# Performance work log

Measured on AMD Instinct MI355X. Metric: run time of the kernel, lower is better.

The kernel has to match this reference:

```python
import jax, jax.numpy as jnp
import numpy as np

# Config constants (mirror NEATConfig)
B = 4096          # population_size
N = 256           # nodes per genome (padded)
E = 4096          # connections per genome (padded)
NUM_INPUTS = 64
NUM_OUTPUTS = 8
NUM_LAYERS = 4    # layers 0..3; layer 0 = inputs


def setup_inputs() -> dict:
    key = jax.random.key(0)
    k_in, k_layer, k_ci, k_co, k_w, k_en = jax.random.split(key, 6)
    inputs = jax.random.normal(k_in, (B, NUM_INPUTS), dtype=jnp.float32)
    # first NUM_INPUTS nodes are input nodes (layer 0); rest in layers 1..NUM_LAYERS-1
    hidden_layers = jax.random.randint(k_layer, (B, N - NUM_INPUTS), 1, NUM_LAYERS, dtype=jnp.int32)
    node_layer = jnp.concatenate(
        [jnp.zeros((B, NUM_INPUTS), dtype=jnp.int32), hidden_layers], axis=1)
    conn_in = jax.random.randint(k_ci, (B, E), 0, N, dtype=jnp.int32)
    conn_out = jax.random.randint(k_co, (B, E), 0, N, dtype=jnp.int32)
    conn_weight = jax.random.normal(k_w, (B, E), dtype=jnp.float32)
    conn_enabled = jax.random.randint(k_en, (B, E), 0, 2) > 0
    return {
        "inputs": inputs,
        "node_layer": node_layer,
        "conn_in": conn_in,
        "conn_out": conn_out,
        "conn_weight": conn_weight,
        "conn_enabled": conn_enabled,
    }


def reference(inputs, node_layer, conn_in, conn_out, conn_weight, conn_enabled):
    """Batched NEAT.forward: layered gather-weight-sum-activate over connection graph.

    inputs:       [B, NUM_INPUTS] float
    node_layer:   [B, N] int  (layer id per node)
    conn_in/out:  [B, E] int  (connection endpoints)
    conn_weight:  [B, E] float
    conn_enabled: [B, E] bool
    returns:      [B, NUM_OUTPUTS]
    """
    b, n = node_layer.shape
    dtype = inputs.dtype
    enabled_f = conn_enabled.astype(dtype)
    batch_idx = jnp.arange(b)[:, None]  # [B,1] for batched scatter

    # node_values init: zeros, inputs written into first NUM_INPUTS slots
    vals = jnp.zeros((b, n), dtype=dtype).at[:, :NUM_INPUTS].set(inputs)

    # per-node count of enabled incoming connections (the `if not incoming: continue` mask)
    in_count = jnp.zeros((b, n), dtype=dtype).at[batch_idx, conn_out].add(enabled_f)

    for layer in range(1, NUM_LAYERS):
        # gather source values, weight, mask disabled -> messages [B,E]
        msgs = jnp.take_along_axis(vals, conn_in, axis=1) * conn_weight * enabled_f
        # sum-aggregate messages per target node [B,N]
        agg = jnp.zeros((b, n), dtype=dtype).at[batch_idx, conn_out].add(msgs)
        upd = jnp.tanh(agg)  # activation_default = tanh
        mask = (node_layer == layer) & (in_count > 0)
        vals = jnp.where(mask, upd, vals)

    return vals[:, NUM_INPUTS:NUM_INPUTS + NUM_OUTPUTS]
```

## Files before the change

### kernel.cpp

```cpp
#include <hip/hip_runtime.h>


#define NN   256
#define NE   4096
#define NIN  64
#define NOUT 8
#define NT   256
#define NWAVE 4

__global__ __launch_bounds__(NT) void neat_fwd(
    const float* __restrict__ inputs,
    const int*   __restrict__ node_layer,
    const int*   __restrict__ conn_in,
    const int*   __restrict__ conn_out,
    const float* __restrict__ conn_w,
    const unsigned char* __restrict__ conn_en,
    float*       __restrict__ out)
{
    const int b    = blockIdx.x;
    const int t    = threadIdx.x;
    const int wave = t >> 6;
    const int lane = t & 63;
    const unsigned long long lmlt = (1ull << lane) - 1ull;

    __shared__ float vals[NN];
    __shared__ float agg[NN];
    __shared__ int   nl_sh[NN];
    __shared__ uint2 edges[NE];
    __shared__ int   wave_cnt[NWAVE][3];
    __shared__ int   wave_base[NWAVE][3];
    __shared__ int   Loff[5];

    const unsigned int* en_w = (const unsigned int*)conn_en;
    bool byte_mode = false;
#pragma unroll
    for (int i = 0; i < 16; ++i) byte_mode |= (en_w[i] > 1u);

    const int nl = node_layer[(size_t)b * NN + t];
    nl_sh[t] = nl;
    vals[t]  = (t < NIN) ? inputs[(size_t)b * NIN + t] : 0.0f;

    const int4*   ci4 = (const int4*)(conn_in  + (size_t)b * NE);
    const int4*   co4 = (const int4*)(conn_out + (size_t)b * NE);
    const float4* w4  = (const float4*)(conn_w  + (size_t)b * NE);

    int4 a0 = ci4[t             ];
    int4 a1 = ci4[t + 1*NT      ];
    int4 a2 = ci4[t + 2*NT      ];
    int4 a3 = ci4[t + 3*NT      ];
    int4 c0 = co4[t             ];
    int4 c1 = co4[t + 1*NT      ];
    int4 c2 = co4[t + 2*NT      ];
    int4 c3 = co4[t + 3*NT      ];
    float4 w0 = w4[t            ];
    float4 w1 = w4[t + 1*NT     ];
    float4 w2 = w4[t + 2*NT     ];
    float4 w3 = w4[t + 3*NT     ];

    unsigned m = 0;
    if (byte_mode) {
        const uchar4* e4 = (const uchar4*)(conn_en + (size_t)b * NE);
        uchar4 e0 = e4[t       ];
        uchar4 e1 = e4[t + 1*NT];
        uchar4 e2 = e4[t + 2*NT];
        uchar4 e3 = e4[t + 3*NT];
        m = (e0.x ? 1u<<0  : 0u) | (e0.y ? 1u<<1  : 0u) | (e0.z ? 1u<<2  : 0u) | (e0.w ? 1u<<3  : 0u)
          | (e1.x ? 1u<<4  : 0u) | (e1.y ? 1u<<5  : 0u) | (e1.z ? 1u<<6  : 0u) | (e1.w ? 1u<<7  : 0u)
          | (e2.x ? 1u<<8  : 0u) | (e2.y ? 1u<<9  : 0u) | (e2.z ? 1u<<10 : 0u) | (e2.w ? 1u<<11 : 0u)
          | (e3.x ? 1u<<12 : 0u) | (e3.y ? 1u<<13 : 0u) | (e3.z ? 1u<<14 : 0u) | (e3.w ? 1u<<15 : 0u);
    } else {
        const int4* e4 = (const int4*)((const int*)conn_en + (size_t)b * NE);
        int4 e0 = e4[t       ];
        int4 e1 = e4[t + 1*NT];
        int4 e2 = e4[t + 2*NT];
        int4 e3 = e4[t + 3*NT];
        m = (e0.x ? 1u<<0  : 0u) | (e0.y ? 1u<<1  : 0u) | (e0.z ? 1u<<2  : 0u) | (e0.w ? 1u<<3  : 0u)
          | (e1.x ? 1u<<4  : 0u) | (e1.y ? 1u<<5  : 0u) | (e1.z ? 1u<<6  : 0u) | (e1.w ? 1u<<7  : 0u)
          | (e2.x ? 1u<<8  : 0u) | (e2.y ? 1u<<9  : 0u) | (e2.z ? 1u<<10 : 0u) | (e2.w ? 1u<<11 : 0u)
          | (e3.x ? 1u<<12 : 0u) | (e3.y ? 1u<<13 : 0u) | (e3.z ? 1u<<14 : 0u) | (e3.w ? 1u<<15 : 0u);
    }
    __syncthreads();

    unsigned keys = 0;
    int c1n = 0, c2n = 0, c3n = 0;
#define KEYSLOT(J, CO) { \
        int kk = nl_sh[(CO)]; \
        kk = ((m >> (J)) & 1u) ? kk : 0; \
        keys |= (unsigned)kk << (2*(J)); \
        c1n += (kk == 1); c2n += (kk == 2); c3n += (kk == 3); }
    KEYSLOT(0,  c0.x) KEYSLOT(1,  c0.y) KEYSLOT(2,  c0.z) KEYSLOT(3,  c0.w)
    KEYSLOT(4,  c1.x) KEYSLOT(5,  c1.y) KEYSLOT(6,  c1.z) KEYSLOT(7,  c1.w)
    KEYSLOT(8,  c2.x) KEYSLOT(9,  c2.y) KEYSLOT(10, c2.z) KEYSLOT(11, c2.w)
    KEYSLOT(12, c3.x) KEYSLOT(13, c3.y) KEYSLOT(14, c3.z) KEYSLOT(15, c3.w)
#undef KEYSLOT

#pragma unroll
    for (int off = 32; off > 0; off >>= 1) {
        c1n += __shfl_down(c1n, off);
        c2n += __shfl_down(c2n, off);
        c3n += __shfl_down(c3n, off);
    }
    if (lane == 0) {
        wave_cnt[wave][0] = c1n;
        wave_cnt[wave][1] = c2n;
        wave_cnt[wave][2] = c3n;
    }
    __syncthreads();

    if (t == 0) {
        int T1 = 0, T2 = 0, T3 = 0;
#pragma unroll
        for (int w = 0; w < NWAVE; ++w) {
            T1 += wave_cnt[w][0]; T2 += wave_cnt[w][1]; T3 += wave_cnt[w][2];
        }
        Loff[1] = 0; Loff[2] = T1; Loff[3] = T1 + T2; Loff[4] = T1 + T2 + T3;
        int r1 = 0, r2 = 0, r3 = 0;
#pragma unroll
        for (int w = 0; w < NWAVE; ++w) {
            wave_base[w][0] = 0       + r1; r1 += wave_cnt[w][0];
            wave_base[w][1] = T1      + r2; r2 += wave_cnt[w][1];
            wave_base[w][2] = T1 + T2 + r3; r3 += wave_cnt[w][2];
        }
    }
    __syncthreads();

    int base1 = wave_base[wave][0];
    int base2 = wave_base[wave][1];
    int base3 = wave_base[wave][2];
#define SCAT(J, CI, CO, W) { \
        int kk = (int)((keys >> (2*(J))) & 3u); \
        unsigned long long B1 = __ballot(kk == 1); \
        unsigned long long B2 = __ballot(kk == 2); \
        unsigned long long B3 = __ballot(kk == 3); \
        if (kk) { \
            unsigned long long bk = (kk == 1) ? B1 : ((kk == 2) ? B2 : B3); \
            int bs = (kk == 1) ? base1 : ((kk == 2) ? base2 : base3); \
            int pos = bs + __popcll(bk & lmlt); \
            edges[pos] = make_uint2(__float_as_uint(W), \
                                    (unsigned)(CI) | ((unsigned)(CO) << 16)); \
        } \
        base1 += __popcll(B1); base2 += __popcll(B2); base3 += __popcll(B3); }
    SCAT(0,  a0.x, c0.x, w0.x) SCAT(1,  a0.y, c0.y, w0.y)
    SCAT(2,  a0.z, c0.z, w0.z) SCAT(3,  a0.w, c0.w, w0.w)
    SCAT(4,  a1.x, c1.x, w1.x) SCAT(5,  a1.y, c1.y, w1.y)
    SCAT(6,  a1.z, c1.z, w1.z) SCAT(7,  a1.w, c1.w, w1.w)
    SCAT(8,  a2.x, c2.x, w2.x) SCAT(9,  a2.y, c2.y, w2.y)
    SCAT(10, a2.z, c2.z, w2.z) SCAT(11, a2.w, c2.w, w2.w)
    SCAT(12, a3.x, c3.x, w3.x) SCAT(13, a3.y, c3.y, w3.y)
    SCAT(14, a3.z, c3.z, w3.z) SCAT(15, a3.w, c3.w, w3.w)
#undef SCAT
    __syncthreads();

#pragma unroll
    for (int L = 1; L < 4; ++L) {
        agg[t] = 0.0f;
        __syncthreads();
        const int s = Loff[L], e = Loff[L + 1];
        for (int p = s + t; p < e; p += NT) {
            uint2 ed = edges[p];
            const int src = (int)(ed.y & 0xFFFFu);
            const int tgt = (int)(ed.y >> 16);
            atomicAdd(&agg[tgt], vals[src] * __uint_as_float(ed.x));
        }
        __syncthreads();
        if (nl == L)
            vals[t] = tanhf(agg[t]);
        __syncthreads();
    }

    if (t < NOUT)
        out[(size_t)b * NOUT + t] = vals[NIN + t];
}

extern "C" void kernel_launch(void* const* d_in, const int* in_sizes, int n_in,
                              void* d_out, int out_size, void* d_ws, size_t ws_size,
                              hipStream_t stream) {
    const float* inputs          = (const float*)d_in[0];
    const int*   node_layer      = (const int*)d_in[1];
    const int*   conn_in         = (const int*)d_in[2];
    const int*   conn_out        = (const int*)d_in[3];
    const float* conn_w          = (const float*)d_in[4];
    const unsigned char* conn_en = (const unsigned char*)d_in[5];
    float* out = (float*)d_out;

    const int B = in_sizes[0] / NIN;
    neat_fwd<<<B, NT, 0, stream>>>(inputs, node_layer, conn_in, conn_out,
                                   conn_w, conn_en, out);
}
```

Measured before the change: 254.4 us.

## Compact shared edge storage to raise occupancy, add register fallback path

Splits the shared edge list into a float weight array and a 16-bit packed index array capped at 2560 entries. It also stores node layers as bytes, which cuts LDS per block so more blocks can be resident (launch bounds now request 8). Block-0 prefix computation is replaced by every thread computing offsets redundantly, which removes a barrier. Per-layer barriers are merged by zeroing agg after the read. When the enabled edge count exceeds the cap, a fallback applies atomics straight from registers, adding code size and register pressure.

```diff
diff --git a/kernel.cpp b/kernel.cpp
--- a/kernel.cpp
+++ b/kernel.cpp
@@ -1,14 +1,15 @@
 #include <hip/hip_runtime.h>
 
 
-#define NN   256
-#define NE   4096
-#define NIN  64
-#define NOUT 8
-#define NT   256
+#define NN    256
+#define NE    4096
+#define NIN   64
+#define NOUT  8
+#define NT    256
 #define NWAVE 4
-
-__global__ __launch_bounds__(NT) void neat_fwd(
+#define CAP   2560
+
+__global__ __launch_bounds__(NT, 8) void neat_fwd(
     const float* __restrict__ inputs,
     const int*   __restrict__ node_layer,
     const int*   __restrict__ conn_in,
@@ -23,13 +24,12 @@
     const int lane = t & 63;
     const unsigned long long lmlt = (1ull << lane) - 1ull;
 
-    __shared__ float vals[NN];
-    __shared__ float agg[NN];
-    __shared__ int   nl_sh[NN];
-    __shared__ uint2 edges[NE];
-    __shared__ int   wave_cnt[NWAVE][3];
-    __shared__ int   wave_base[NWAVE][3];
-    __shared__ int   Loff[5];
+    __shared__ float          vals[NN];
+    __shared__ float          agg[NN];
+    __shared__ unsigned char  nl_sh[NN];
+    __shared__ float          ew[CAP];
+    __shared__ unsigned short ep[CAP];
+    __shared__ int            wave_cnt[NWAVE][3];
 
     const unsigned int* en_w = (const unsigned int*)conn_en;
     bool byte_mode = false;
@@ -37,25 +37,26 @@
     for (int i = 0; i < 16; ++i) byte_mode |= (en_w[i] > 1u);
 
     const int nl = node_layer[(size_t)b * NN + t];
-    nl_sh[t] = nl;
+    nl_sh[t] = (unsigned char)nl;
     vals[t]  = (t < NIN) ? inputs[(size_t)b * NIN + t] : 0.0f;
+    agg[t]   = 0.0f;
 
     const int4*   ci4 = (const int4*)(conn_in  + (size_t)b * NE);
     const int4*   co4 = (const int4*)(conn_out + (size_t)b * NE);
     const float4* w4  = (const float4*)(conn_w  + (size_t)b * NE);
 
-    int4 a0 = ci4[t             ];
-    int4 a1 = ci4[t + 1*NT      ];
-    int4 a2 = ci4[t + 2*NT      ];
-    int4 a3 = ci4[t + 3*NT      ];
-    int4 c0 = co4[t             ];
-    int4 c1 = co4[t + 1*NT      ];
-    int4 c2 = co4[t + 2*NT      ];
-    int4 c3 = co4[t + 3*NT      ];
-    float4 w0 = w4[t            ];
-    float4 w1 = w4[t + 1*NT     ];
-    float4 w2 = w4[t + 2*NT     ];
-    float4 w3 = w4[t + 3*NT     ];
+    int4 a0 = ci4[t       ];
+    int4 a1 = ci4[t + 1*NT];
+    int4 a2 = ci4[t + 2*NT];
+    int4 a3 = ci4[t + 3*NT];
+    int4 c0 = co4[t       ];
+    int4 c1 = co4[t + 1*NT];
+    int4 c2 = co4[t + 2*NT];
+    int4 c3 = co4[t + 3*NT];
+    float4 w0 = w4[t       ];
+    float4 w1 = w4[t + 1*NT];
+    float4 w2 = w4[t + 2*NT];
+    float4 w3 = w4[t + 3*NT];
 
     unsigned m = 0;
     if (byte_mode) {
@@ -84,7 +85,7 @@
     unsigned keys = 0;
     int c1n = 0, c2n = 0, c3n = 0;
 #define KEYSLOT(J, CO) { \
-        int kk = nl_sh[(CO)]; \
+        int kk = (int)nl_sh[(CO)]; \
         kk = ((m >> (J)) & 1u) ? kk : 0; \
         keys |= (unsigned)kk << (2*(J)); \
         c1n += (kk == 1); c2n += (kk == 2); c3n += (kk == 3); }
@@ -107,26 +108,19 @@
     }
     __syncthreads();
 
-    if (t == 0) {
-        int T1 = 0, T2 = 0, T3 = 0;
-#pragma unroll
-        for (int w = 0; w < NWAVE; ++w) {
-            T1 += wave_cnt[w][0]; T2 += wave_cnt[w][1]; T3 += wave_cnt[w][2];
-        }
-        Loff[1] = 0; Loff[2] = T1; Loff[3] = T1 + T2; Loff[4] = T1 + T2 + T3;
-        int r1 = 0, r2 = 0, r3 = 0;
-#pragma unroll
-        for (int w = 0; w < NWAVE; ++w) {
-            wave_base[w][0] = 0       + r1; r1 += wave_cnt[w][0];
-            wave_base[w][1] = T1      + r2; r2 += wave_cnt[w][1];
-            wave_base[w][2] = T1 + T2 + r3; r3 += wave_cnt[w][2];
-        }
-    }
-    __syncthreads();
-
-    int base1 = wave_base[wave][0];
-    int base2 = wave_base[wave][1];
-    int base3 = wave_base[wave][2];
+    int T1 = 0, T2 = 0, T3 = 0, p1 = 0, p2 = 0, p3 = 0;
+#pragma unroll
+    for (int w = 0; w < NWAVE; ++w) {
+        const int x = wave_cnt[w][0], y = wave_cnt[w][1], z = wave_cnt[w][2];
+        if (w < wave) { p1 += x; p2 += y; p3 += z; }
+        T1 += x; T2 += y; T3 += z;
+    }
+    const int total = T1 + T2 + T3;
+
+    if (total <= CAP) {
+        int base1 = p1;
+        int base2 = T1 + p2;
+        int base3 = T1 + T2 + p3;
 #define SCAT(J, CI, CO, W) { \
         int kk = (int)((keys >> (2*(J))) & 3u); \
         unsigned long long B1 = __ballot(kk == 1); \
@@ -136,40 +130,62 @@
             unsigned long long bk = (kk == 1) ? B1 : ((kk == 2) ? B2 : B3); \
             int bs = (kk == 1) ? base1 : ((kk == 2) ? base2 : base3); \
             int pos = bs + __popcll(bk & lmlt); \
-            edges[pos] = make_uint2(__float_as_uint(W), \
-                                    (unsigned)(CI) | ((unsigned)(CO) << 16)); \
+            ew[pos] = (W); \
+            ep[pos] = (unsigned short)((unsigned)(CI) | ((unsigned)(CO) << 8)); \
         } \
         base1 += __popcll(B1); base2 += __popcll(B2); base3 += __popcll(B3); }
-    SCAT(0,  a0.x, c0.x, w0.x) SCAT(1,  a0.y, c0.y, w0.y)
-    SCAT(2,  a0.z, c0.z, w0.z) SCAT(3,  a0.w, c0.w, w0.w)
-    SCAT(4,  a1.x, c1.x, w1.x) SCAT(5,  a1.y, c1.y, w1.y)
-    SCAT(6,  a1.z, c1.z, w1.z) SCAT(7,  a1.w, c1.w, w1.w)
-    SCAT(8,  a2.x, c2.x, w2.x) SCAT(9,  a2.y, c2.y, w2.y)
-    SCAT(10, a2.z, c2.z, w2.z) SCAT(11, a2.w, c2.w, w2.w)
-    SCAT(12, a3.x, c3.x, w3.x) SCAT(13, a3.y, c3.y, w3.y)
-    SCAT(14, a3.z, c3.z, w3.z) SCAT(15, a3.w, c3.w, w3.w)
+        SCAT(0,  a0.x, c0.x, w0.x) SCAT(1,  a0.y, c0.y, w0.y)
+        SCAT(2,  a0.z, c0.z, w0.z) SCAT(3,  a0.w, c0.w, w0.w)
+        SCAT(4,  a1.x, c1.x, w1.x) SCAT(5,  a1.y, c1.y, w1.y)
+        SCAT(6,  a1.z, c1.z, w1.z) SCAT(7,  a1.w, c1.w, w1.w)
+        SCAT(8,  a2.x, c2.x, w2.x) SCAT(9,  a2.y, c2.y, w2.y)
+        SCAT(10, a2.z, c2.z, w2.z) SCAT(11, a2.w, c2.w, w2.w)
+        SCAT(12, a3.x, c3.x, w3.x) SCAT(13, a3.y, c3.y, w3.y)
+        SCAT(14, a3.z, c3.z, w3.z) SCAT(15, a3.w, c3.w, w3.w)
 #undef SCAT
-    __syncthreads();
-
-#pragma unroll
-    for (int L = 1; L < 4; ++L) {
-        agg[t] = 0.0f;
         __syncthreads();
-        const int s = Loff[L], e = Loff[L + 1];
-        for (int p = s + t; p < e; p += NT) {
-            uint2 ed = edges[p];
-            const int src = (int)(ed.y & 0xFFFFu);
-            const int tgt = (int)(ed.y >> 16);
-            atomicAdd(&agg[tgt], vals[src] * __uint_as_float(ed.x));
+
+        float vreg = vals[t];
+#pragma unroll
+        for (int L = 1; L < 4; ++L) {
+            const int s = (L == 1) ? 0  : ((L == 2) ? T1 : T1 + T2);
+            const int e = (L == 1) ? T1 : ((L == 2) ? T1 + T2 : total);
+            for (int p = s + t; p < e; p += NT) {
+                const unsigned pk = ep[p];
+                atomicAdd(&agg[pk >> 8], vals[pk & 0xFFu] * ew[p]);
+            }
+            __syncthreads();
+            const float u = agg[t];
+            if (nl == L) { vreg = tanhf(u); vals[t] = vreg; }
+            agg[t] = 0.0f;
+            if (L < 3) __syncthreads();
         }
-        __syncthreads();
-        if (nl == L)
-            vals[t] = tanhf(agg[t]);
-        __syncthreads();
-    }
-
-    if (t < NOUT)
-        out[(size_t)b * NOUT + t] = vals[NIN + t];
+        if (t >= NIN && t < NIN + NOUT)
+            out[(size_t)b * NOUT + (t - NIN)] = vreg;
+    } else {
+        float vreg = vals[t];
+#pragma unroll
+        for (int L = 1; L < 4; ++L) {
+#define FB(J, CI, CO, W) \
+            if (((keys >> (2*(J))) & 3u) == (unsigned)L) atomicAdd(&agg[(CO)], vals[(CI)] * (W));
+            FB(0,  a0.x, c0.x, w0.x) FB(1,  a0.y, c0.y, w0.y)
+            FB(2,  a0.z, c0.z, w0.z) FB(3,  a0.w, c0.w, w0.w)
+            FB(4,  a1.x, c1.x, w1.x) FB(5,  a1.y, c1.y, w1.y)
+            FB(6,  a1.z, c1.z, w1.z) FB(7,  a1.w, c1.w, w1.w)
+            FB(8,  a2.x, c2.x, w2.x) FB(9,  a2.y, c2.y, w2.y)
+            FB(10, a2.z, c2.z, w2.z) FB(11, a2.w, c2.w, w2.w)
+            FB(12, a3.x, c3.x, w3.x) FB(13, a3.y, c3.y, w3.y)
+            FB(14, a3.z, c3.z, w3.z) FB(15, a3.w, c3.w, w3.w)
+#undef FB
+            __syncthreads();
+            const float u = agg[t];
+            if (nl == L) { vreg = tanhf(u); vals[t] = vreg; }
+            agg[t] = 0.0f;
+            if (L < 3) __syncthreads();
+        }
+        if (t >= NIN && t < NIN + NOUT)
+            out[(size_t)b * NOUT + (t - NIN)] = vreg;
+    }
 }
 
 extern "C" void kernel_launch(void* const* d_in, const int* in_sizes, int n_in,
```

After: 318.5 us. 1.25x slower.
